# Performance work log

Measured on AMD Instinct MI355X. Metric: run time of the kernel, lower is better.

The kernel has to match this reference:

```python
import jax, jax.numpy as jnp
import numpy as np

QK_K = 256          # values per Q4_K super-block
TYPE_SIZE = 144     # bytes per Q4_K block: 2 (d fp16) + 2 (dmin fp16) + 12 (scales) + 128 (qs)
OUT_FEATURES = 8192
IN_FEATURES = 8192
BATCH = 256


def setup_inputs() -> dict:
    rng = np.random.default_rng(0)
    n_blocks = OUT_FEATURES * IN_FEATURES // QK_K
    # Pack valid little-endian fp16 super-block scales into raw bytes (as a GGUF file would store them).
    d16 = rng.uniform(0.001, 0.01, size=(n_blocks,)).astype(np.float16)
    dmin16 = rng.uniform(0.0005, 0.005, size=(n_blocks,)).astype(np.float16)
    scales = rng.integers(0, 256, size=(n_blocks, 12), dtype=np.uint8)  # packed 6-bit sub-scales/mins
    qs = rng.integers(0, 256, size=(n_blocks, 128), dtype=np.uint8)     # 4-bit quants, 2 per byte
    blocks = np.concatenate(
        [d16.view(np.uint8).reshape(n_blocks, 2),
         dmin16.view(np.uint8).reshape(n_blocks, 2),
         scales, qs], axis=1)  # [n_blocks, 144] uint8
    key = jax.random.key(0)
    kx, kb = jax.random.split(key)
    x = jax.random.normal(kx, (BATCH, IN_FEATURES), dtype=jnp.float32)
    bias = jax.random.normal(kb, (OUT_FEATURES,), dtype=jnp.float32) * 0.01
    return {"x": x, "qweight": jnp.asarray(blocks), "bias": bias}


def _bitcast_f16(bytes2):
    # bytes2: [n, 2] uint8 (little-endian) -> [n] float32
    n = bytes2.shape[0]
    return jax.lax.bitcast_convert_type(bytes2.reshape(n, 1, 2), jnp.float16).reshape(n).astype(jnp.float32)


def _get_scale_min(scales):
    # scales: [n, 12] uint8 -> 8 six-bit sub-block scales and mins, each [n, 8]
    n = scales.shape[0]
    s = scales.reshape(n, 3, 4)
    d_, m_, md = s[:, 0], s[:, 1], s[:, 2]  # each [n, 4]
    sc = jnp.concatenate([d_ & 63, (md & 15) | ((d_ >> 2) & 48)], axis=-1)
    mn = jnp.concatenate([m_ & 63, (md >> 4) | ((m_ >> 2) & 48)], axis=-1)
    return sc, mn


def dequantize_q4_k(blocks):
    # blocks: [n_blocks, 144] uint8 -> [n_blocks, 256] float32
    n = blocks.shape[0]
    d = _bitcast_f16(blocks[:, 0:2])       # [n]
    dmin = _bitcast_f16(blocks[:, 2:4])    # [n]
    sc, mn = _get_scale_min(blocks[:, 4:16])
    dl = (d[:, None] * sc.astype(jnp.float32)).reshape(n, 8, 1)   # per-sub-block scale
    ml = (dmin[:, None] * mn.astype(jnp.float32)).reshape(n, 8, 1)  # per-sub-block min
    qs = blocks[:, 16:].reshape(n, 4, 1, 32)                       # 128 bytes
    shift = jnp.array([0, 4], dtype=jnp.uint8).reshape(1, 1, 2, 1)
    q = ((qs >> shift) & 15).reshape(n, 8, 32).astype(jnp.float32)  # low then high nibbles
    return (dl * q - ml).reshape(n, QK_K)


def reference(x, qweight, bias):
    qweight = qweight.astype(jnp.uint8)
    W = dequantize_q4_k(qweight).reshape(OUT_FEATURES, IN_FEATURES)  # [out, in]
    return x @ W.T + bias  # F.linear(x, W, bias)
```

## Files before the change

kernel.cpp:

```cpp
#include <hip/hip_runtime.h>
#include <hip/hip_fp16.h>

typedef __bf16 bf16x8 __attribute__((ext_vector_type(8)));
typedef float floatx16 __attribute__((ext_vector_type(16)));
typedef unsigned int uint;
typedef unsigned short ushort;
typedef uint  uintx4  __attribute__((ext_vector_type(4)));
typedef float floatx4 __attribute__((ext_vector_type(4)));

constexpr int Mdim = 256, Ndim = 8192, Kdim = 8192;
constexpr int BN = 64, BK = 64, KSPLIT = 4;
constexpr int KS = Kdim / KSPLIT;
constexpr int NT = KS / BK;
constexpr int KB = Kdim / 256;

union U8 { uint u[4]; bf16x8 v; };

__device__ __forceinline__ uint cvtpk(float lo, float hi) {
  uint r; asm("v_cvt_pk_bf16_f32 %0, %1, %2" : "=v"(r) : "v"(lo), "v"(hi));
  return r;
}

template <typename T>
__device__ __forceinline__ T gld(const void* p) {
  return *(const __attribute__((address_space(1))) T*)p;
}

__device__ __forceinline__ int bswz(int row, int ch) {
  return row * 64 + ((ch ^ (row & 7)) << 3);
}

template<bool PRE>
__global__ __launch_bounds__(256, 2)
void q4k_gemm(const float* __restrict__ x, const bf16x8* __restrict__ xbf,
              const int* __restrict__ qw, const float* __restrict__ bias,
              float* __restrict__ out)
{
  __shared__ ushort Bb[2][BN * 64];

  const int tid = threadIdx.x;
  const int bid = blockIdx.x;
  const int l  = (bid & 7) * 64 + (bid >> 3);
  const int nb = l >> 2;
  const int ks = l & 3;
  const int n0 = nb * BN;
  const int ks8 = ks * (KS >> 8);

  const int sr = tid >> 2;
  const int sq = tid & 3;

  const int lane = tid & 63;
  const int wave = tid >> 6;
  const int mb0  = wave * 2;
  const int brow = lane & 31;
  const int bco  = lane >> 5;

  const int* bp0 = qw + (n0 + sr) * (KB * 144);
  const bf16x8* xA0 = PRE ? (xbf + ((mb0    ) * 512 + ks * 128) * 64 + lane) : nullptr;
  const bf16x8* xA1 = PRE ? (xbf + ((mb0 + 1) * 512 + ks * 128) * 64 + lane) : nullptr;

  uintx4 R[4][2];
  uintx4 Mdd[2], M0[2], M1[2], M2[2];
  U8 pqL, pqH;
  bf16x8 aA[8], aB[8];
  floatx16 acc00 = {}, acc01 = {}, acc10 = {}, acc11 = {};

  auto gloadB = [&](int s2, int rs, int ms, bool meta) {
    const int* bp = bp0 + (ks8 + (s2 >> 2)) * 144;
    const int* qp = bp + 16 + (s2 & 3) * 32 + sq * 8;
    R[rs][0] = gld<uintx4>(qp);
    R[rs][1] = gld<uintx4>(qp + 4);
    if (meta) {
      Mdd[ms] = gld<uintx4>(bp);
      M0[ms]  = gld<uintx4>(bp + 4);
      M1[ms]  = gld<uintx4>(bp + 8);
      M2[ms]  = gld<uintx4>(bp + 12);
    }
  };

  auto gloadA = [&](int t, bf16x8 (&A)[8]) {
    if constexpr (PRE) {
      const int f = t * 4 * 64;
      #pragma unroll
      for (int kk = 0; kk < 4; ++kk) {
        A[kk]     = gld<bf16x8>(xA0 + f + kk * 64);
        A[4 + kk] = gld<bf16x8>(xA1 + f + kk * 64);
      }
    } else {
      const int kg = ks * KS + t * BK + bco * 8;
      #pragma unroll
      for (int kk = 0; kk < 4; ++kk) {
        const float* fA = x + (mb0 * 32 + brow) * Kdim + kg + kk * 16;
        const float* fB = x + ((mb0 + 1) * 32 + brow) * Kdim + kg + kk * 16;
        const floatx4 p0 = gld<floatx4>(fA), p1 = gld<floatx4>(fA + 4);
        const floatx4 q0 = gld<floatx4>(fB), q1 = gld<floatx4>(fB + 4);
        U8 ua, ub;
        ua.u[0] = cvtpk(p0.x, p0.y); ua.u[1] = cvtpk(p0.z, p0.w);
        ua.u[2] = cvtpk(p1.x, p1.y); ua.u[3] = cvtpk(p1.z, p1.w);
        ub.u[0] = cvtpk(q0.x, q0.y); ub.u[1] = cvtpk(q0.z, q0.w);
        ub.u[2] = cvtpk(q1.x, q1.y); ub.u[3] = cvtpk(q1.z, q1.w);
        A[kk] = ua.v; A[4 + kk] = ub.v;
      }
    }
  };

  auto dequant = [&](int c, int rs, int ms) {
    const uintx4 dd = Mdd[ms];
    const float d  = __half2float(__ushort_as_half((ushort)((dd.x & 255u) | ((dd.y & 255u) << 8))));
    const float dm = __half2float(__ushort_as_half((ushort)((dd.z & 255u) | ((dd.w & 255u) << 8))));
    const uintx4 s0 = M0[ms], s1 = M1[ms], s2 = M2[ms];
    uint scA, scB, mnA, mnB;
    if (c == 0)      { scA = s0.x & 63u; scB = s0.y & 63u; mnA = s1.x & 63u; mnB = s1.y & 63u; }
    else if (c == 1) { scA = s0.z & 63u; scB = s0.w & 63u; mnA = s1.z & 63u; mnB = s1.w & 63u; }
    else if (c == 2) {
      scA = (s2.x & 15u) | ((s0.x >> 2) & 48u); scB = (s2.y & 15u) | ((s0.y >> 2) & 48u);
      mnA = (s2.x >> 4)  | ((s1.x >> 2) & 48u); mnB = (s2.y >> 4)  | ((s1.y >> 2) & 48u);
    } else {
      scA = (s2.z & 15u) | ((s0.z >> 2) & 48u); scB = (s2.w & 15u) | ((s0.w >> 2) & 48u);
      mnA = (s2.z >> 4)  | ((s1.z >> 2) & 48u); mnB = (s2.w >> 4)  | ((s1.w >> 2) & 48u);
    }
    const float dlA = d * (float)scA, mlA = dm * (float)mnA;
    const float dlB = d * (float)scB, mlB = dm * (float)mnB;
    float wl[8], wh[8];
    #pragma unroll
    for (int h = 0; h < 2; ++h) {
      const uintx4 qv = R[rs][h];
      wl[h*4+0] = fmaf(dlA, (float)(qv.x & 15u), -mlA);
      wl[h*4+1] = fmaf(dlA, (float)(qv.y & 15u), -mlA);
      wl[h*4+2] = fmaf(dlA, (float)(qv.z & 15u), -mlA);
      wl[h*4+3] = fmaf(dlA, (float)(qv.w & 15u), -mlA);
      wh[h*4+0] = fmaf(dlB, (float)(qv.x >> 4), -mlB);
      wh[h*4+1] = fmaf(dlB, (float)(qv.y >> 4), -mlB);
      wh[h*4+2] = fmaf(dlB, (float)(qv.z >> 4), -mlB);
      wh[h*4+3] = fmaf(dlB, (float)(qv.w >> 4), -mlB);
    }
    #pragma unroll
    for (int p = 0; p < 4; ++p) {
      pqL.u[p] = cvtpk(wl[2*p], wl[2*p+1]);
      pqH.u[p] = cvtpk(wh[2*p], wh[2*p+1]);
    }
  };

  auto bwrite = [&](int bufi) {
    *(bf16x8*)&Bb[bufi][bswz(sr, sq)]     = pqL.v;
    *(bf16x8*)&Bb[bufi][bswz(sr, 4 + sq)] = pqH.v;
  };

  auto mstep = [&](int bufi, const bf16x8 (&A)[8]) {
    #pragma unroll
    for (int kk = 0; kk < 4; ++kk) {
      const bf16x8 bq0 = *(const bf16x8*)&Bb[bufi][bswz(brow,      kk * 2 + bco)];
      const bf16x8 bq1 = *(const bf16x8*)&Bb[bufi][bswz(brow + 32, kk * 2 + bco)];
      acc00 = __builtin_amdgcn_mfma_f32_32x32x16_bf16(A[kk],     bq0, acc00, 0, 0, 0);
      acc01 = __builtin_amdgcn_mfma_f32_32x32x16_bf16(A[kk],     bq1, acc01, 0, 0, 0);
      acc10 = __builtin_amdgcn_mfma_f32_32x32x16_bf16(A[4 + kk], bq0, acc10, 0, 0, 0);
      acc11 = __builtin_amdgcn_mfma_f32_32x32x16_bf16(A[4 + kk], bq1, acc11, 0, 0, 0);
    }
  };

  gloadB(0, 0, 0, true);
  gloadB(1, 1, 0, false);
  gloadB(2, 2, 0, false);
  gloadB(3, 3, 0, false);
  gloadA(0, aA);
  gloadA(1, aB);
  dequant(0, 0, 0);
  bwrite(0);
  asm volatile("s_waitcnt lgkmcnt(0)" ::: "memory");
  __builtin_amdgcn_s_barrier();
  __builtin_amdgcn_sched_barrier(0);

  #define PH(u, CUR) {                                                       \
    const int s_ = base + (u);                                               \
    if (s_ + 4 < NT) gloadB(s_ + 4, (u) & 3, (((u) + 4) >> 2) & 1,           \
                            (((u) + 4) & 3) == 0);                           \
    if (s_ + 1 < NT) {                                                       \
      dequant(((u) + 1) & 3, ((u) + 1) & 3, (((u) + 1) >> 2) & 1);           \
      bwrite(((u) + 1) & 1);                                                 \
    }                                                                        \
    __builtin_amdgcn_s_setprio(1);                                           \
    mstep((u) & 1, CUR);                                                     \
    __builtin_amdgcn_s_setprio(0);                                           \
    if (s_ + 2 < NT) gloadA(s_ + 2, CUR);                                    \
    asm volatile("s_waitcnt lgkmcnt(0)" ::: "memory");                       \
    __builtin_amdgcn_s_barrier();                                            \
    __builtin_amdgcn_sched_barrier(0);                                       \
  }

  for (int base = 0; base < NT; base += 8) {
    PH(0, aA) PH(1, aB) PH(2, aA) PH(3, aB)
    PH(4, aA) PH(5, aB) PH(6, aA) PH(7, aB)
  }
  #undef PH

  const int gn0 = n0 + (lane & 31);
  const int gn1 = gn0 + 32;
  const float bv0 = (ks == 0) ? bias[gn0] : 0.0f;
  const float bv1 = (ks == 0) ? bias[gn1] : 0.0f;
  const int mrow = wave * 64 + 4 * (lane >> 5);
  #pragma unroll
  for (int r = 0; r < 16; ++r) {
    const int m = mrow + (r & 3) + 8 * (r >> 2);
    atomicAdd(&out[m * Ndim + gn0], acc00[r] + bv0);
    atomicAdd(&out[m * Ndim + gn1], acc01[r] + bv1);
    atomicAdd(&out[(m + 32) * Ndim + gn0], acc10[r] + bv0);
    atomicAdd(&out[(m + 32) * Ndim + gn1], acc11[r] + bv1);
  }
}

template<bool DOCVT>
__global__ __launch_bounds__(256)
void prep(const float* __restrict__ x, uintx4* __restrict__ xb,
          floatx4* __restrict__ out)
{
  const int gid = blockIdx.x * 256 + threadIdx.x;
  out[gid * 2]     = floatx4{0.f, 0.f, 0.f, 0.f};
  out[gid * 2 + 1] = floatx4{0.f, 0.f, 0.f, 0.f};
  if (DOCVT) {
    const int lane = gid & 63;
    const int m = ((gid >> 15) * 32) + (lane & 31);
    const int k = (((gid >> 6) & 511) * 16) + (lane >> 5) * 8;
    const floatx4 f0 = gld<floatx4>(x + m * Kdim + k);
    const floatx4 f1 = gld<floatx4>(x + m * Kdim + k + 4);
    uintx4 st;
    st.x = cvtpk(f0.x, f0.y); st.y = cvtpk(f0.z, f0.w);
    st.z = cvtpk(f1.x, f1.y); st.w = cvtpk(f1.z, f1.w);
    xb[gid] = st;
  }
}

extern "C" void kernel_launch(void* const* d_in, const int* in_sizes, int n_in,
                              void* d_out, int out_size, void* d_ws, size_t ws_size,
                              hipStream_t stream) {
  (void)in_sizes; (void)n_in; (void)out_size;
  const float* x    = (const float*)d_in[0];
  const int*   qw   = (const int*)d_in[1];
  const float* bias = (const float*)d_in[2];
  float* out = (float*)d_out;

  const size_t need = (size_t)Mdim * Kdim * 2;
  if (ws_size >= need) {
    prep<true><<<1024, 256, 0, stream>>>(x, (uintx4*)d_ws, (floatx4*)out);
    q4k_gemm<true><<<512, 256, 0, stream>>>(x, (const bf16x8*)d_ws, qw, bias, out);
  } else {
    prep<false><<<1024, 256, 0, stream>>>(x, nullptr, (floatx4*)out);
    q4k_gemm<false><<<512, 256, 0, stream>>>(x, nullptr, qw, bias, out);
  }
}
```

Before: 71.14 us.

## Double threads per block, splitting N tile across wave pairs

Raises the GEMM block from 256 to 512 threads. Each wave pair now shares the M rows and splits the 64-column N tile into two 32-column halves, so each wave holds two accumulators instead of four. Each thread dequantizes half as many weights per stage. The goal is more waves in flight to hide load and dequant latency and less per-thread register pressure. In exchange, every A fragment is now loaded by two waves, which doubles A traffic, and the barrier now synchronises more waves.

After: 85.67 us. 1.2x slower.

```diff
diff --git a/kernel.cpp b/kernel.cpp
--- a/kernel.cpp
+++ b/kernel.cpp
@@ -6,6 +6,7 @@
 typedef unsigned int uint;
 typedef unsigned short ushort;
 typedef uint  uintx4  __attribute__((ext_vector_type(4)));
+typedef uint  uintx2  __attribute__((ext_vector_type(2)));
 typedef float floatx4 __attribute__((ext_vector_type(4)));
 
 constexpr int Mdim = 256, Ndim = 8192, Kdim = 8192;
@@ -14,7 +15,7 @@
 constexpr int NT = KS / BK;
 constexpr int KB = Kdim / 256;
 
-union U8 { uint u[4]; bf16x8 v; };
+union U4 { uint u[2]; uintx2 v; };
 
 __device__ __forceinline__ uint cvtpk(float lo, float hi) {
   uint r; asm("v_cvt_pk_bf16_f32 %0, %1, %2" : "=v"(r) : "v"(lo), "v"(hi));
@@ -31,7 +32,7 @@
 }
 
 template<bool PRE>
-__global__ __launch_bounds__(256, 2)
+__global__ __launch_bounds__(512, 2)
 void q4k_gemm(const float* __restrict__ x, const bf16x8* __restrict__ xbf,
               const int* __restrict__ qw, const float* __restrict__ bias,
               float* __restrict__ out)
@@ -46,12 +47,13 @@
   const int n0 = nb * BN;
   const int ks8 = ks * (KS >> 8);
 
-  const int sr = tid >> 2;
-  const int sq = tid & 3;
+  const int sr = tid >> 3;
+  const int sq = tid & 7;
 
   const int lane = tid & 63;
   const int wave = tid >> 6;
-  const int mb0  = wave * 2;
+  const int wn   = wave & 1;
+  const int mb0  = (wave >> 1) * 2;
   const int brow = lane & 31;
   const int bco  = lane >> 5;
 
@@ -59,17 +61,16 @@
   const bf16x8* xA0 = PRE ? (xbf + ((mb0    ) * 512 + ks * 128) * 64 + lane) : nullptr;
   const bf16x8* xA1 = PRE ? (xbf + ((mb0 + 1) * 512 + ks * 128) * 64 + lane) : nullptr;
 
-  uintx4 R[4][2];
+  uintx4 R[4];
   uintx4 Mdd[2], M0[2], M1[2], M2[2];
-  U8 pqL, pqH;
+  uintx2 pqL, pqH;
   bf16x8 aA[8], aB[8];
-  floatx16 acc00 = {}, acc01 = {}, acc10 = {}, acc11 = {};
+  floatx16 acc00 = {}, acc10 = {};
 
   auto gloadB = [&](int s2, int rs, int ms, bool meta) {
     const int* bp = bp0 + (ks8 + (s2 >> 2)) * 144;
-    const int* qp = bp + 16 + (s2 & 3) * 32 + sq * 8;
-    R[rs][0] = gld<uintx4>(qp);
-    R[rs][1] = gld<uintx4>(qp + 4);
+    const int* qp = bp + 16 + (s2 & 3) * 32 + sq * 4;
+    R[rs] = gld<uintx4>(qp);
     if (meta) {
       Mdd[ms] = gld<uintx4>(bp);
       M0[ms]  = gld<uintx4>(bp + 4);
@@ -94,7 +95,7 @@
         const float* fB = x + ((mb0 + 1) * 32 + brow) * Kdim + kg + kk * 16;
         const floatx4 p0 = gld<floatx4>(fA), p1 = gld<floatx4>(fA + 4);
         const floatx4 q0 = gld<floatx4>(fB), q1 = gld<floatx4>(fB + 4);
-        U8 ua, ub;
+        union { uint u[4]; bf16x8 v; } ua, ub;
         ua.u[0] = cvtpk(p0.x, p0.y); ua.u[1] = cvtpk(p0.z, p0.w);
         ua.u[2] = cvtpk(p1.x, p1.y); ua.u[3] = cvtpk(p1.z, p1.w);
         ub.u[0] = cvtpk(q0.x, q0.y); ub.u[1] = cvtpk(q0.z, q0.w);
@@ -121,40 +122,30 @@
     }
     const float dlA = d * (float)scA, mlA = dm * (float)mnA;
     const float dlB = d * (float)scB, mlB = dm * (float)mnB;
-    float wl[8], wh[8];
-    #pragma unroll
-    for (int h = 0; h < 2; ++h) {
-      const uintx4 qv = R[rs][h];
-      wl[h*4+0] = fmaf(dlA, (float)(qv.x & 15u), -mlA);
-      wl[h*4+1] = fmaf(dlA, (float)(qv.y & 15u), -mlA);
-      wl[h*4+2] = fmaf(dlA, (float)(qv.z & 15u), -mlA);
-      wl[h*4+3] = fmaf(dlA, (float)(qv.w & 15u), -mlA);
-      wh[h*4+0] = fmaf(dlB, (float)(qv.x >> 4), -mlB);
-      wh[h*4+1] = fmaf(dlB, (float)(qv.y >> 4), -mlB);
-      wh[h*4+2] = fmaf(dlB, (float)(qv.z >> 4), -mlB);
-      wh[h*4+3] = fmaf(dlB, (float)(qv.w >> 4), -mlB);
-    }
-    #pragma unroll
-    for (int p = 0; p < 4; ++p) {
-      pqL.u[p] = cvtpk(wl[2*p], wl[2*p+1]);
-      pqH.u[p] = cvtpk(wh[2*p], wh[2*p+1]);
-    }
+    const uintx4 qv = R[rs];
+    const float w0 = fmaf(dlA, (float)(qv.x & 15u), -mlA);
+    const float w1 = fmaf(dlA, (float)(qv.y & 15u), -mlA);
+    const float w2 = fmaf(dlA, (float)(qv.z & 15u), -mlA);
+    const float w3 = fmaf(dlA, (float)(qv.w & 15u), -mlA);
+    const float h0 = fmaf(dlB, (float)(qv.x >> 4), -mlB);
+    const float h1 = fmaf(dlB, (float)(qv.y >> 4), -mlB);
+    const float h2 = fmaf(dlB, (float)(qv.z >> 4), -mlB);
+    const float h3 = fmaf(dlB, (float)(qv.w >> 4), -mlB);
+    pqL.x = cvtpk(w0, w1); pqL.y = cvtpk(w2, w3);
+    pqH.x = cvtpk(h0, h1); pqH.y = cvtpk(h2, h3);
   };
 
   auto bwrite = [&](int bufi) {
-    *(bf16x8*)&Bb[bufi][bswz(sr, sq)]     = pqL.v;
-    *(bf16x8*)&Bb[bufi][bswz(sr, 4 + sq)] = pqH.v;
+    *(uintx2*)&Bb[bufi][bswz(sr, (sq >> 1))     + (sq & 1) * 4] = pqL;
+    *(uintx2*)&Bb[bufi][bswz(sr, 4 + (sq >> 1)) + (sq & 1) * 4] = pqH;
   };
 
   auto mstep = [&](int bufi, const bf16x8 (&A)[8]) {
     #pragma unroll
     for (int kk = 0; kk < 4; ++kk) {
-      const bf16x8 bq0 = *(const bf16x8*)&Bb[bufi][bswz(brow,      kk * 2 + bco)];
-      const bf16x8 bq1 = *(const bf16x8*)&Bb[bufi][bswz(brow + 32, kk * 2 + bco)];
-      acc00 = __builtin_amdgcn_mfma_f32_32x32x16_bf16(A[kk],     bq0, acc00, 0, 0, 0);
-      acc01 = __builtin_amdgcn_mfma_f32_32x32x16_bf16(A[kk],     bq1, acc01, 0, 0, 0);
-      acc10 = __builtin_amdgcn_mfma_f32_32x32x16_bf16(A[4 + kk], bq0, acc10, 0, 0, 0);
-      acc11 = __builtin_amdgcn_mfma_f32_32x32x16_bf16(A[4 + kk], bq1, acc11, 0, 0, 0);
+      const bf16x8 bq = *(const bf16x8*)&Bb[bufi][bswz(wn * 32 + brow, kk * 2 + bco)];
+      acc00 = __builtin_amdgcn_mfma_f32_32x32x16_bf16(A[kk],     bq, acc00, 0, 0, 0);
+      acc10 = __builtin_amdgcn_mfma_f32_32x32x16_bf16(A[4 + kk], bq, acc10, 0, 0, 0);
     }
   };
 
@@ -193,18 +184,14 @@
   }
   #undef PH
 
-  const int gn0 = n0 + (lane & 31);
-  const int gn1 = gn0 + 32;
-  const float bv0 = (ks == 0) ? bias[gn0] : 0.0f;
-  const float bv1 = (ks == 0) ? bias[gn1] : 0.0f;
-  const int mrow = wave * 64 + 4 * (lane >> 5);
+  const int gn = n0 + wn * 32 + (lane & 31);
+  const float bv = (ks == 0) ? bias[gn] : 0.0f;
+  const int mrow = (wave >> 1) * 64 + 4 * (lane >> 5);
   #pragma unroll
   for (int r = 0; r < 16; ++r) {
     const int m = mrow + (r & 3) + 8 * (r >> 2);
-    atomicAdd(&out[m * Ndim + gn0], acc00[r] + bv0);
-    atomicAdd(&out[m * Ndim + gn1], acc01[r] + bv1);
-    atomicAdd(&out[(m + 32) * Ndim + gn0], acc10[r] + bv0);
-    atomicAdd(&out[(m + 32) * Ndim + gn1], acc11[r] + bv1);
+    atomicAdd(&out[m * Ndim + gn], acc00[r] + bv);
+    atomicAdd(&out[(m + 32) * Ndim + gn], acc10[r] + bv);
   }
 }
 
@@ -241,9 +228,9 @@
   const size_t need = (size_t)Mdim * Kdim * 2;
   if (ws_size >= need) {
     prep<true><<<1024, 256, 0, stream>>>(x, (uintx4*)d_ws, (floatx4*)out);
-    q4k_gemm<true><<<512, 256, 0, stream>>>(x, (const bf16x8*)d_ws, qw, bias, out);
+    q4k_gemm<true><<<512, 512, 0, stream>>>(x, (const bf16x8*)d_ws, qw, bias, out);
   } else {
     prep<false><<<1024, 256, 0, stream>>>(x, nullptr, (floatx4*)out);
-    q4k_gemm<false><<<512, 256, 0, stream>>>(x, nullptr, qw, bias, out);
-  }
-}
+    q4k_gemm<false><<<512, 512, 0, stream>>>(x, nullptr, qw, bias, out);
+  }
+}
```

## Double the K step per barrier to halve LDS synchronisation count

Applied to the files above, without the earlier changes.

Each pipeline phase now covers two 64-wide K sub-tiles (128 K per barrier): the LDS B buffer grows to 128 columns with a 16-way XOR swizzle, two dequant/bwrite pairs fill it, and two mstep calls consume it. Metadata loads are split into a separate mload scheduled every other phase. The aim is to halve the number of s_waitcnt and barrier stalls per K range. In exchange it doubles LDS use and may raise register pressure, which could hurt occupancy at two blocks per CU.

After: 70.92 us. About the same (-0.3%).

```diff
diff --git a/kernel.cpp b/kernel.cpp
--- a/kernel.cpp
+++ b/kernel.cpp
@@ -9,9 +9,9 @@
 typedef float floatx4 __attribute__((ext_vector_type(4)));
 
 constexpr int Mdim = 256, Ndim = 8192, Kdim = 8192;
-constexpr int BN = 64, BK = 64, KSPLIT = 4;
+constexpr int BN = 64, KSPLIT = 4;
 constexpr int KS = Kdim / KSPLIT;
-constexpr int NT = KS / BK;
+constexpr int NT = KS / 64;
 constexpr int KB = Kdim / 256;
 
 union U8 { uint u[4]; bf16x8 v; };
@@ -27,7 +27,7 @@
 }
 
 __device__ __forceinline__ int bswz(int row, int ch) {
-  return row * 64 + ((ch ^ (row & 7)) << 3);
+  return row * 128 + ((ch ^ (row & 15)) << 3);
 }
 
 template<bool PRE>
@@ -36,7 +36,7 @@
               const int* __restrict__ qw, const float* __restrict__ bias,
               float* __restrict__ out)
 {
-  __shared__ ushort Bb[2][BN * 64];
+  __shared__ ushort Bb[2][BN * 128];
 
   const int tid = threadIdx.x;
   const int bid = blockIdx.x;
@@ -65,17 +65,18 @@
   bf16x8 aA[8], aB[8];
   floatx16 acc00 = {}, acc01 = {}, acc10 = {}, acc11 = {};
 
-  auto gloadB = [&](int s2, int rs, int ms, bool meta) {
-    const int* bp = bp0 + (ks8 + (s2 >> 2)) * 144;
-    const int* qp = bp + 16 + (s2 & 3) * 32 + sq * 8;
+  auto gloadB = [&](int s2, int rs) {
+    const int* qp = bp0 + (ks8 + (s2 >> 2)) * 144 + 16 + (s2 & 3) * 32 + sq * 8;
     R[rs][0] = gld<uintx4>(qp);
     R[rs][1] = gld<uintx4>(qp + 4);
-    if (meta) {
-      Mdd[ms] = gld<uintx4>(bp);
-      M0[ms]  = gld<uintx4>(bp + 4);
-      M1[ms]  = gld<uintx4>(bp + 8);
-      M2[ms]  = gld<uintx4>(bp + 12);
-    }
+  };
+
+  auto mload = [&](int sbrel, int ms) {
+    const int* bp = bp0 + (ks8 + sbrel) * 144;
+    Mdd[ms] = gld<uintx4>(bp);
+    M0[ms]  = gld<uintx4>(bp + 4);
+    M1[ms]  = gld<uintx4>(bp + 8);
+    M2[ms]  = gld<uintx4>(bp + 12);
   };
 
   auto gloadA = [&](int t, bf16x8 (&A)[8]) {
@@ -87,7 +88,7 @@
         A[4 + kk] = gld<bf16x8>(xA1 + f + kk * 64);
       }
     } else {
-      const int kg = ks * KS + t * BK + bco * 8;
+      const int kg = ks * KS + t * 64 + bco * 8;
       #pragma unroll
       for (int kk = 0; kk < 4; ++kk) {
         const float* fA = x + (mb0 * 32 + brow) * Kdim + kg + kk * 16;
@@ -141,16 +142,16 @@
     }
   };
 
-  auto bwrite = [&](int bufi) {
-    *(bf16x8*)&Bb[bufi][bswz(sr, sq)]     = pqL.v;
-    *(bf16x8*)&Bb[bufi][bswz(sr, 4 + sq)] = pqH.v;
-  };
-
-  auto mstep = [&](int bufi, const bf16x8 (&A)[8]) {
+  auto bwrite = [&](int bufi, int h) {
+    *(bf16x8*)&Bb[bufi][bswz(sr, h * 8 + sq)]     = pqL.v;
+    *(bf16x8*)&Bb[bufi][bswz(sr, h * 8 + 4 + sq)] = pqH.v;
+  };
+
+  auto mstep = [&](int bufi, int h, const bf16x8 (&A)[8]) {
     #pragma unroll
     for (int kk = 0; kk < 4; ++kk) {
-      const bf16x8 bq0 = *(const bf16x8*)&Bb[bufi][bswz(brow,      kk * 2 + bco)];
-      const bf16x8 bq1 = *(const bf16x8*)&Bb[bufi][bswz(brow + 32, kk * 2 + bco)];
+      const bf16x8 bq0 = *(const bf16x8*)&Bb[bufi][bswz(brow,      h * 8 + kk * 2 + bco)];
+      const bf16x8 bq1 = *(const bf16x8*)&Bb[bufi][bswz(brow + 32, h * 8 + kk * 2 + bco)];
       acc00 = __builtin_amdgcn_mfma_f32_32x32x16_bf16(A[kk],     bq0, acc00, 0, 0, 0);
       acc01 = __builtin_amdgcn_mfma_f32_32x32x16_bf16(A[kk],     bq1, acc01, 0, 0, 0);
       acc10 = __builtin_amdgcn_mfma_f32_32x32x16_bf16(A[4 + kk], bq0, acc10, 0, 0, 0);
@@ -158,40 +159,48 @@
     }
   };
 
-  gloadB(0, 0, 0, true);
-  gloadB(1, 1, 0, false);
-  gloadB(2, 2, 0, false);
-  gloadB(3, 3, 0, false);
-  gloadA(0, aA);
-  gloadA(1, aB);
-  dequant(0, 0, 0);
-  bwrite(0);
+  mload(0, 0); mload(1, 1);
+  gloadB(0, 0); gloadB(1, 1); gloadB(2, 2); gloadB(3, 3);
+  gloadA(0, aA); gloadA(1, aB);
+  dequant(0, 0, 0); bwrite(0, 0);
+  dequant(1, 1, 0); bwrite(0, 1);
   asm volatile("s_waitcnt lgkmcnt(0)" ::: "memory");
   __builtin_amdgcn_s_barrier();
   __builtin_amdgcn_sched_barrier(0);
 
-  #define PH(u, CUR) {                                                       \
-    const int s_ = base + (u);                                               \
-    if (s_ + 4 < NT) gloadB(s_ + 4, (u) & 3, (((u) + 4) >> 2) & 1,           \
-                            (((u) + 4) & 3) == 0);                           \
-    if (s_ + 1 < NT) {                                                       \
-      dequant(((u) + 1) & 3, ((u) + 1) & 3, (((u) + 1) >> 2) & 1);           \
-      bwrite(((u) + 1) & 1);                                                 \
-    }                                                                        \
+  #define MLOADJ(j)                                                          \
+    if ((j) == 1) { const int sb_ = B / 2 + 2; if (sb_ < 8) mload(sb_, 0); } \
+    else if ((j) == 3) { const int sb_ = B / 2 + 3; if (sb_ < 8) mload(sb_, 1); }
+
+  #define PH2(j) {                                                           \
+    const int p_ = B + (j);                                                  \
+    const int s1_ = 2 * p_ + 2, s2_ = 2 * p_ + 3;                            \
+    if (s1_ < NT) { dequant((2*(j)+2)&3, (2*(j)+2)&3, (((j)+1)>>1)&1);       \
+                    bwrite(((j)&1)^1, 0); }                                  \
+    if (s2_ < NT) { dequant((2*(j)+3)&3, (2*(j)+3)&3, (((j)+1)>>1)&1);       \
+                    bwrite(((j)&1)^1, 1); }                                  \
+    if (s1_ + 2 < NT) gloadB(s1_ + 2, (2*(j)+4)&3);                          \
+    if (s2_ + 2 < NT) gloadB(s2_ + 2, (2*(j)+5)&3);                          \
+    MLOADJ(j)                                                                \
     __builtin_amdgcn_s_setprio(1);                                           \
-    mstep((u) & 1, CUR);                                                     \
+    mstep((j)&1, 0, aA);                                                     \
     __builtin_amdgcn_s_setprio(0);                                           \
-    if (s_ + 2 < NT) gloadA(s_ + 2, CUR);                                    \
+    if (s1_ < NT) gloadA(s1_, aA);                                           \
+    __builtin_amdgcn_s_setprio(1);                                           \
+    mstep((j)&1, 1, aB);                                                     \
+    __builtin_amdgcn_s_setprio(0);                                           \
+    if (s2_ < NT) gloadA(s2_, aB);                                           \
     asm volatile("s_waitcnt lgkmcnt(0)" ::: "memory");                       \
     __builtin_amdgcn_s_barrier();                                            \
     __builtin_amdgcn_sched_barrier(0);                                       \
   }
 
-  for (int base = 0; base < NT; base += 8) {
-    PH(0, aA) PH(1, aB) PH(2, aA) PH(3, aB)
-    PH(4, aA) PH(5, aB) PH(6, aA) PH(7, aB)
-  }
-  #undef PH
+  for (int i = 0; i < 4; ++i) {
+    const int B = i * 4;
+    PH2(0) PH2(1) PH2(2) PH2(3)
+  }
+  #undef PH2
+  #undef MLOADJ
 
   const int gn0 = n0 + (lane & 31);
   const int gn1 = gn0 + 32;
```

## Stage raw Q4_K blocks into LDS via async DMA and dequantize in MFMA loop

Applied to the files above, without the earlier changes.

Replaces per-thread global loads of quantized weights plus a dequantize-then-write-bf16-to-LDS step with direct global_load_lds DMA of whole 144-byte Q4_K super-blocks into a padded, XOR-swizzled LDS layout, one super-block per stage, double-buffered. Each wave then reads the packed nibbles and metadata from LDS and dequantizes to bf16 in registers right before the MFMAs, removing the bf16 LDS write and some VGPR staging. The barrier count drops to one per super-block (four k-tiles), with vmcnt waits for synchronisation. The cost is redundant dequantization, since each wave now dequantizes the same B tile that was previously done once per block, plus more complex address math in the DMA index computation.

Measured after the change: 85.50 us. +20.2%, slower.

```diff
diff --git a/kernel.cpp b/kernel.cpp
--- a/kernel.cpp
+++ b/kernel.cpp
@@ -9,10 +9,12 @@
 typedef float floatx4 __attribute__((ext_vector_type(4)));
 
 constexpr int Mdim = 256, Ndim = 8192, Kdim = 8192;
-constexpr int BN = 64, BK = 64, KSPLIT = 4;
+constexpr int BN = 64, KSPLIT = 4;
 constexpr int KS = Kdim / KSPLIT;
-constexpr int NT = KS / BK;
+constexpr int NT = KS / 64;
 constexpr int KB = Kdim / 256;
+constexpr int ROWI = 148;
+constexpr int SLOTI = 64 * ROWI;
 
 union U8 { uint u[4]; bf16x8 v; };
 
@@ -20,15 +22,16 @@
   uint r; asm("v_cvt_pk_bf16_f32 %0, %1, %2" : "=v"(r) : "v"(lo), "v"(hi));
   return r;
 }
-
 template <typename T>
 __device__ __forceinline__ T gld(const void* p) {
   return *(const __attribute__((address_space(1))) T*)p;
 }
-
-__device__ __forceinline__ int bswz(int row, int ch) {
-  return row * 64 + ((ch ^ (row & 7)) << 3);
-}
+__device__ __forceinline__ void glds16(const void* g, void* l) {
+  __builtin_amdgcn_global_load_lds(
+      (const __attribute__((address_space(1))) uint*)g,
+      (__attribute__((address_space(3))) uint*)l, 16, 0, 0);
+}
+#define WAITVM(n) asm volatile("s_waitcnt vmcnt(" #n ")" ::: "memory")
 
 template<bool PRE>
 __global__ __launch_bounds__(256, 2)
@@ -36,7 +39,7 @@
               const int* __restrict__ qw, const float* __restrict__ bias,
               float* __restrict__ out)
 {
-  __shared__ ushort Bb[2][BN * 64];
+  __shared__ __align__(16) int Qs[2 * SLOTI];
 
   const int tid = threadIdx.x;
   const int bid = blockIdx.x;
@@ -46,36 +49,36 @@
   const int n0 = nb * BN;
   const int ks8 = ks * (KS >> 8);
 
-  const int sr = tid >> 2;
-  const int sq = tid & 3;
-
   const int lane = tid & 63;
   const int wave = tid >> 6;
   const int mb0  = wave * 2;
   const int brow = lane & 31;
   const int bco  = lane >> 5;
-
-  const int* bp0 = qw + (n0 + sr) * (KB * 144);
+  const int lxor = ((bco << 1) ^ (((brow >> 3) & 3) << 1));
+
+  const char* qwb = (const char*)qw;
   const bf16x8* xA0 = PRE ? (xbf + ((mb0    ) * 512 + ks * 128) * 64 + lane) : nullptr;
   const bf16x8* xA1 = PRE ? (xbf + ((mb0 + 1) * 512 + ks * 128) * 64 + lane) : nullptr;
 
-  uintx4 R[4][2];
-  uintx4 Mdd[2], M0[2], M1[2], M2[2];
-  U8 pqL, pqH;
   bf16x8 aA[8], aB[8];
   floatx16 acc00 = {}, acc01 = {}, acc10 = {}, acc11 = {};
-
-  auto gloadB = [&](int s2, int rs, int ms, bool meta) {
-    const int* bp = bp0 + (ks8 + (s2 >> 2)) * 144;
-    const int* qp = bp + 16 + (s2 & 3) * 32 + sq * 8;
-    R[rs][0] = gld<uintx4>(qp);
-    R[rs][1] = gld<uintx4>(qp + 4);
-    if (meta) {
-      Mdd[ms] = gld<uintx4>(bp);
-      M0[ms]  = gld<uintx4>(bp + 4);
-      M1[ms]  = gld<uintx4>(bp + 8);
-      M2[ms]  = gld<uintx4>(bp + 12);
-    }
+  float d0, dm0, d1, dm1;
+  uintx4 s0r0, s1r0, s2r0, s0r1, s1r1, s2r1;
+
+  auto dmaJ = [&](int j, int sbAbs, int slot) {
+    const int i = j * 64 + lane;
+    const int seg = (i * 56680) >> 21;
+    const int rem = i - seg * 37;
+    const int g = (rem < 4) ? rem
+                : (rem == 36) ? 0
+                : 4 + ((rem - 4) ^ (((seg >> 3) & 3) << 1));
+    const char* src = qwb + (size_t)(((n0 + seg) * KB + sbAbs) * 576 + g * 16);
+    glds16((const void*)src, (void*)((char*)Qs + slot * (SLOTI * 4) + j * 1024));
+  };
+  auto stageSB = [&](int sbAbs, int slot) {
+    #pragma unroll
+    for (int q = 0; q < 9; ++q) dmaJ(q * 4 + wave, sbAbs, slot);
+    if (wave == 0) dmaJ(36, sbAbs, slot);
   };
 
   auto gloadA = [&](int t, bf16x8 (&A)[8]) {
@@ -87,7 +90,7 @@
         A[4 + kk] = gld<bf16x8>(xA1 + f + kk * 64);
       }
     } else {
-      const int kg = ks * KS + t * BK + bco * 8;
+      const int kg = ks * KS + t * 64 + bco * 8;
       #pragma unroll
       for (int kk = 0; kk < 4; ++kk) {
         const float* fA = x + (mb0 * 32 + brow) * Kdim + kg + kk * 16;
@@ -104,94 +107,104 @@
     }
   };
 
-  auto dequant = [&](int c, int rs, int ms) {
-    const uintx4 dd = Mdd[ms];
-    const float d  = __half2float(__ushort_as_half((ushort)((dd.x & 255u) | ((dd.y & 255u) << 8))));
-    const float dm = __half2float(__ushort_as_half((ushort)((dd.z & 255u) | ((dd.w & 255u) << 8))));
-    const uintx4 s0 = M0[ms], s1 = M1[ms], s2 = M2[ms];
-    uint scA, scB, mnA, mnB;
-    if (c == 0)      { scA = s0.x & 63u; scB = s0.y & 63u; mnA = s1.x & 63u; mnB = s1.y & 63u; }
-    else if (c == 1) { scA = s0.z & 63u; scB = s0.w & 63u; mnA = s1.z & 63u; mnB = s1.w & 63u; }
-    else if (c == 2) {
-      scA = (s2.x & 15u) | ((s0.x >> 2) & 48u); scB = (s2.y & 15u) | ((s0.y >> 2) & 48u);
-      mnA = (s2.x >> 4)  | ((s1.x >> 2) & 48u); mnB = (s2.y >> 4)  | ((s1.y >> 2) & 48u);
+  auto loadMeta = [&](int slot) {
+    const int b0 = slot * SLOTI + brow * ROWI;
+    const int b1 = b0 + 32 * ROWI;
+    const uintx4 dd0 = *(const uintx4*)&Qs[b0];
+    s0r0 = *(const uintx4*)&Qs[b0 + 4];
+    s1r0 = *(const uintx4*)&Qs[b0 + 8];
+    s2r0 = *(const uintx4*)&Qs[b0 + 12];
+    const uintx4 dd1 = *(const uintx4*)&Qs[b1];
+    s0r1 = *(const uintx4*)&Qs[b1 + 4];
+    s1r1 = *(const uintx4*)&Qs[b1 + 8];
+    s2r1 = *(const uintx4*)&Qs[b1 + 12];
+    d0  = __half2float(__ushort_as_half((ushort)((dd0.x & 255u) | ((dd0.y & 255u) << 8))));
+    dm0 = __half2float(__ushort_as_half((ushort)((dd0.z & 255u) | ((dd0.w & 255u) << 8))));
+    d1  = __half2float(__ushort_as_half((ushort)((dd1.x & 255u) | ((dd1.y & 255u) << 8))));
+    dm1 = __half2float(__ushort_as_half((ushort)((dd1.z & 255u) | ((dd1.w & 255u) << 8))));
+  };
+
+  auto mstepD = [&](int T, int slot, const bf16x8 (&A)[8]) {
+    const int c = T & 3;
+    uint scA0, scB0, mnA0, mnB0, scA1, scB1, mnA1, mnB1;
+    if (c == 0) {
+      scA0 = s0r0.x & 63u; scB0 = s0r0.y & 63u; mnA0 = s1r0.x & 63u; mnB0 = s1r0.y & 63u;
+      scA1 = s0r1.x & 63u; scB1 = s0r1.y & 63u; mnA1 = s1r1.x & 63u; mnB1 = s1r1.y & 63u;
+    } else if (c == 1) {
+      scA0 = s0r0.z & 63u; scB0 = s0r0.w & 63u; mnA0 = s1r0.z & 63u; mnB0 = s1r0.w & 63u;
+      scA1 = s0r1.z & 63u; scB1 = s0r1.w & 63u; mnA1 = s1r1.z & 63u; mnB1 = s1r1.w & 63u;
+    } else if (c == 2) {
+      scA0 = (s2r0.x & 15u) | ((s0r0.x >> 2) & 48u); scB0 = (s2r0.y & 15u) | ((s0r0.y >> 2) & 48u);
+      mnA0 = (s2r0.x >> 4)  | ((s1r0.x >> 2) & 48u); mnB0 = (s2r0.y >> 4)  | ((s1r0.y >> 2) & 48u);
+      scA1 = (s2r1.x & 15u) | ((s0r1.x >> 2) & 48u); scB1 = (s2r1.y & 15u) | ((s0r1.y >> 2) & 48u);
+      mnA1 = (s2r1.x >> 4)  | ((s1r1.x >> 2) & 48u); mnB1 = (s2r1.y >> 4)  | ((s1r1.y >> 2) & 48u);
     } else {
-      scA = (s2.z & 15u) | ((s0.z >> 2) & 48u); scB = (s2.w & 15u) | ((s0.w >> 2) & 48u);
-      mnA = (s2.z >> 4)  | ((s1.z >> 2) & 48u); mnB = (s2.w >> 4)  | ((s1.w >> 2) & 48u);
+      scA0 = (s2r0.z & 15u) | ((s0r0.z >> 2) & 48u); scB0 = (s2r0.w & 15u) | ((s0r0.w >> 2) & 48u);
+      mnA0 = (s2r0.z >> 4)  | ((s1r0.z >> 2) & 48u); mnB0 = (s2r0.w >> 4)  | ((s1r0.w >> 2) & 48u);
+      scA1 = (s2r1.z & 15u) | ((s0r1.z >> 2) & 48u); scB1 = (s2r1.w & 15u) | ((s0r1.w >> 2) & 48u);
+      mnA1 = (s2r1.z >> 4)  | ((s1r1.z >> 2) & 48u); mnB1 = (s2r1.w >> 4)  | ((s1r1.w >> 2) & 48u);
     }
-    const float dlA = d * (float)scA, mlA = dm * (float)mnA;
-    const float dlB = d * (float)scB, mlB = dm * (float)mnB;
-    float wl[8], wh[8];
-    #pragma unroll
-    for (int h = 0; h < 2; ++h) {
-      const uintx4 qv = R[rs][h];
-      wl[h*4+0] = fmaf(dlA, (float)(qv.x & 15u), -mlA);
-      wl[h*4+1] = fmaf(dlA, (float)(qv.y & 15u), -mlA);
-      wl[h*4+2] = fmaf(dlA, (float)(qv.z & 15u), -mlA);
-      wl[h*4+3] = fmaf(dlA, (float)(qv.w & 15u), -mlA);
-      wh[h*4+0] = fmaf(dlB, (float)(qv.x >> 4), -mlB);
-      wh[h*4+1] = fmaf(dlB, (float)(qv.y >> 4), -mlB);
-      wh[h*4+2] = fmaf(dlB, (float)(qv.z >> 4), -mlB);
-      wh[h*4+3] = fmaf(dlB, (float)(qv.w >> 4), -mlB);
-    }
-    #pragma unroll
-    for (int p = 0; p < 4; ++p) {
-      pqL.u[p] = cvtpk(wl[2*p], wl[2*p+1]);
-      pqH.u[p] = cvtpk(wh[2*p], wh[2*p+1]);
-    }
-  };
-
-  auto bwrite = [&](int bufi) {
-    *(bf16x8*)&Bb[bufi][bswz(sr, sq)]     = pqL.v;
-    *(bf16x8*)&Bb[bufi][bswz(sr, 4 + sq)] = pqH.v;
-  };
-
-  auto mstep = [&](int bufi, const bf16x8 (&A)[8]) {
+    const float dlA0 = d0 * (float)scA0, mlA0 = dm0 * (float)mnA0;
+    const float dlB0 = d0 * (float)scB0, mlB0 = dm0 * (float)mnB0;
+    const float dlA1 = d1 * (float)scA1, mlA1 = dm1 * (float)mnA1;
+    const float dlB1 = d1 * (float)scB1, mlB1 = dm1 * (float)mnB1;
+    const int qb0 = slot * SLOTI + brow * ROWI + 16;
+    const int qb1 = qb0 + 32 * ROWI;
     #pragma unroll
     for (int kk = 0; kk < 4; ++kk) {
-      const bf16x8 bq0 = *(const bf16x8*)&Bb[bufi][bswz(brow,      kk * 2 + bco)];
-      const bf16x8 bq1 = *(const bf16x8*)&Bb[bufi][bswz(brow + 32, kk * 2 + bco)];
-      acc00 = __builtin_amdgcn_mfma_f32_32x32x16_bf16(A[kk],     bq0, acc00, 0, 0, 0);
-      acc01 = __builtin_amdgcn_mfma_f32_32x32x16_bf16(A[kk],     bq1, acc01, 0, 0, 0);
-      acc10 = __builtin_amdgcn_mfma_f32_32x32x16_bf16(A[4 + kk], bq0, acc10, 0, 0, 0);
-      acc11 = __builtin_amdgcn_mfma_f32_32x32x16_bf16(A[4 + kk], bq1, acc11, 0, 0, 0);
+      const int xc = (c * 8 + (kk & 1) * 4) ^ lxor;
+      const uintx4 qa0 = *(const uintx4*)&Qs[qb0 + 4 * xc];
+      const uintx4 qa1 = *(const uintx4*)&Qs[qb0 + 4 * xc + 4];
+      const uintx4 qc0 = *(const uintx4*)&Qs[qb1 + 4 * xc];
+      const uintx4 qc1 = *(const uintx4*)&Qs[qb1 + 4 * xc + 4];
+      const bool lo = (kk < 2);
+      const float dl0 = lo ? dlA0 : dlB0, ml0 = lo ? mlA0 : mlB0;
+      const float dl1 = lo ? dlA1 : dlB1, ml1 = lo ? mlA1 : mlB1;
+      U8 f0, f1;
+      #pragma unroll
+      for (int h = 0; h < 2; ++h) {
+        const uintx4 va = h ? qa1 : qa0;
+        const uintx4 vc = h ? qc1 : qc0;
+        const float a0 = fmaf(dl0, (float)(lo ? (va.x & 15u) : (va.x >> 4)), -ml0);
+        const float a1 = fmaf(dl0, (float)(lo ? (va.y & 15u) : (va.y >> 4)), -ml0);
+        const float a2 = fmaf(dl0, (float)(lo ? (va.z & 15u) : (va.z >> 4)), -ml0);
+        const float a3 = fmaf(dl0, (float)(lo ? (va.w & 15u) : (va.w >> 4)), -ml0);
+        const float c0 = fmaf(dl1, (float)(lo ? (vc.x & 15u) : (vc.x >> 4)), -ml1);
+        const float c1 = fmaf(dl1, (float)(lo ? (vc.y & 15u) : (vc.y >> 4)), -ml1);
+        const float c2 = fmaf(dl1, (float)(lo ? (vc.z & 15u) : (vc.z >> 4)), -ml1);
+        const float c3 = fmaf(dl1, (float)(lo ? (vc.w & 15u) : (vc.w >> 4)), -ml1);
+        f0.u[h * 2]     = cvtpk(a0, a1); f0.u[h * 2 + 1] = cvtpk(a2, a3);
+        f1.u[h * 2]     = cvtpk(c0, c1); f1.u[h * 2 + 1] = cvtpk(c2, c3);
+      }
+      acc00 = __builtin_amdgcn_mfma_f32_32x32x16_bf16(A[kk],     f0.v, acc00, 0, 0, 0);
+      acc01 = __builtin_amdgcn_mfma_f32_32x32x16_bf16(A[kk],     f1.v, acc01, 0, 0, 0);
+      acc10 = __builtin_amdgcn_mfma_f32_32x32x16_bf16(A[4 + kk], f0.v, acc10, 0, 0, 0);
+      acc11 = __builtin_amdgcn_mfma_f32_32x32x16_bf16(A[4 + kk], f1.v, acc11, 0, 0, 0);
     }
   };
 
-  gloadB(0, 0, 0, true);
-  gloadB(1, 1, 0, false);
-  gloadB(2, 2, 0, false);
-  gloadB(3, 3, 0, false);
+  stageSB(ks8, 0);
   gloadA(0, aA);
   gloadA(1, aB);
-  dequant(0, 0, 0);
-  bwrite(0);
-  asm volatile("s_waitcnt lgkmcnt(0)" ::: "memory");
+  if constexpr (PRE) { WAITVM(16); } else { WAITVM(32); }
   __builtin_amdgcn_s_barrier();
   __builtin_amdgcn_sched_barrier(0);
 
-  #define PH(u, CUR) {                                                       \
-    const int s_ = base + (u);                                               \
-    if (s_ + 4 < NT) gloadB(s_ + 4, (u) & 3, (((u) + 4) >> 2) & 1,           \
-                            (((u) + 4) & 3) == 0);                           \
-    if (s_ + 1 < NT) {                                                       \
-      dequant(((u) + 1) & 3, ((u) + 1) & 3, (((u) + 1) >> 2) & 1);           \
-      bwrite(((u) + 1) & 1);                                                 \
-    }                                                                        \
-    __builtin_amdgcn_s_setprio(1);                                           \
-    mstep((u) & 1, CUR);                                                     \
-    __builtin_amdgcn_s_setprio(0);                                           \
-    if (s_ + 2 < NT) gloadA(s_ + 2, CUR);                                    \
+  #define SST(S) {                                                           \
+    if ((S) < 7) stageSB(ks8 + (S) + 1, ((S) + 1) & 1);                      \
+    loadMeta((S) & 1);                                                       \
+    mstepD(4*(S) + 0, (S) & 1, aA); if (4*(S) + 2 < NT) gloadA(4*(S) + 2, aA); \
+    mstepD(4*(S) + 1, (S) & 1, aB); if (4*(S) + 3 < NT) gloadA(4*(S) + 3, aB); \
+    mstepD(4*(S) + 2, (S) & 1, aA); if (4*(S) + 4 < NT) gloadA(4*(S) + 4, aA); \
+    mstepD(4*(S) + 3, (S) & 1, aB); if (4*(S) + 5 < NT) gloadA(4*(S) + 5, aB); \
+    if ((S) < 7) { if constexpr (PRE) { WAITVM(32); } else { WAITVM(63); } } \
     asm volatile("s_waitcnt lgkmcnt(0)" ::: "memory");                       \
     __builtin_amdgcn_s_barrier();                                            \
     __builtin_amdgcn_sched_barrier(0);                                       \
   }
 
-  for (int base = 0; base < NT; base += 8) {
-    PH(0, aA) PH(1, aB) PH(2, aA) PH(3, aB)
-    PH(4, aA) PH(5, aB) PH(6, aA) PH(7, aB)
-  }
-  #undef PH
+  SST(0) SST(1) SST(2) SST(3) SST(4) SST(5) SST(6) SST(7)
+  #undef SST
 
   const int gn0 = n0 + (lane & 31);
   const int gn1 = gn0 + 32;
```
